# Optimization experiments

Measured on AMD Instinct MI355X. Metric: run time of the kernel, lower is better.

## Reference

```python
import jax, jax.numpy as jnp
import numpy as np
import math

N_USER = 50000
N_ITEM = 50000
E_PER = 400000
F_IN = 128
F_OUT = 128
H = 4
D = F_OUT // H  # 32
NUM_ET = 2  # edge types: 0 = user->item, 1 = item->user


def setup_inputs() -> dict:
    key = jax.random.key(0)
    ks = jax.random.split(key, 16)
    s = 0.05  # weight scale to keep activations tame
    return {
        "x_user": jax.random.normal(ks[0], (N_USER, F_IN), jnp.float32),
        "x_item": jax.random.normal(ks[1], (N_ITEM, F_IN), jnp.float32),
        "W_kqv_user": jax.random.normal(ks[2], (F_IN, 3 * F_OUT), jnp.float32) * s,
        "b_kqv_user": jax.random.normal(ks[3], (3 * F_OUT,), jnp.float32) * s,
        "W_kqv_item": jax.random.normal(ks[4], (F_IN, 3 * F_OUT), jnp.float32) * s,
        "b_kqv_item": jax.random.normal(ks[5], (3 * F_OUT,), jnp.float32) * s,
        "Wk_rel": jax.random.normal(ks[6], (H * NUM_ET, D, D), jnp.float32) * s,
        "Wv_rel": jax.random.normal(ks[7], (H * NUM_ET, D, D), jnp.float32) * s,
        "W_out_user": jax.random.normal(ks[8], (F_OUT, F_OUT), jnp.float32) * s,
        "b_out_user": jax.random.normal(ks[9], (F_OUT,), jnp.float32) * s,
        "W_out_item": jax.random.normal(ks[10], (F_OUT, F_OUT), jnp.float32) * s,
        "b_out_item": jax.random.normal(ks[11], (F_OUT,), jnp.float32) * s,
        "skip_user": jnp.ones((1,), jnp.float32),
        "skip_item": jnp.ones((1,), jnp.float32),
        "p_rel_ui": jnp.ones((H,), jnp.float32),
        "p_rel_iu": jnp.ones((H,), jnp.float32),
        "edge_ui": jax.random.randint(ks[12], (2, E_PER), 0, N_USER, dtype=jnp.int32),
        "edge_iu": jax.random.randint(ks[13], (2, E_PER), 0, N_ITEM, dtype=jnp.int32),
    }


def _kqv(x, W, b):
    o = x @ W + b  # [N, 3F]
    k, q, v = o[:, :F_OUT], o[:, F_OUT:2 * F_OUT], o[:, 2 * F_OUT:]
    return (k.reshape(-1, H, D), q.reshape(-1, H, D), v.reshape(-1, H, D))


def _rel(x, Wrel, et):
    # HeteroLinear with type index h*NUM_ET + et per head (is_sorted layout)
    W = Wrel[jnp.arange(H) * NUM_ET + et]  # [H, D, D]
    return jnp.einsum('nhd,hde->nhe', x, W)


def reference(x_user, x_item, W_kqv_user, b_kqv_user, W_kqv_item, b_kqv_item,
              Wk_rel, Wv_rel, W_out_user, b_out_user, W_out_item, b_out_item,
              skip_user, skip_item, p_rel_ui, p_rel_iu, edge_ui, edge_iu):
    ku, qu, vu = _kqv(x_user, W_kqv_user, b_kqv_user)
    ki, qi, vi = _kqv(x_item, W_kqv_item, b_kqv_item)

    # per-edge-type relation transform of K/V (grouped GEMM by head x edge-type)
    k0, v0 = _rel(ku, Wk_rel, 0), _rel(vu, Wv_rel, 0)  # src of user->item
    k1, v1 = _rel(ki, Wk_rel, 1), _rel(vi, Wv_rel, 1)  # src of item->user

    q_all = jnp.concatenate([qu, qi], 0)  # dst offsets: user=0, item=N_USER
    n_tot = N_USER + N_ITEM

    src0, dst0 = edge_ui[0], edge_ui[1] + N_USER
    src1, dst1 = edge_iu[0], edge_iu[1]

    kj = jnp.concatenate([k0[src0], k1[src1]], 0)  # [E, H, D]
    vj = jnp.concatenate([v0[src0], v1[src1]], 0)  # [E, H, D]
    dst = jnp.concatenate([dst0, dst1], 0)         # [E]
    p = jnp.concatenate([jnp.broadcast_to(p_rel_ui, (E_PER, H)),
                         jnp.broadcast_to(p_rel_iu, (E_PER, H))], 0)

    qe = q_all[dst]                                  # [E, H, D]
    alpha = (qe * kj).sum(-1) * p / math.sqrt(D)     # [E, H]

    # segment softmax over destination nodes (PyG softmax: max-shift, +1e-16)
    amax = jax.ops.segment_max(alpha, dst, num_segments=n_tot)
    a = jnp.exp(alpha - amax[dst])
    denom = jax.ops.segment_sum(a, dst, num_segments=n_tot)
    a = a / (denom[dst] + 1e-16)

    out = jax.ops.segment_sum(vj * a[:, :, None], dst, num_segments=n_tot)
    out = out.reshape(n_tot, F_OUT)
    out_u, out_i = out[:N_USER], out[N_USER:]

    g = lambda t: jax.nn.gelu(t, approximate=False)
    a_u = g(out_u) @ W_out_user + b_out_user
    a_i = g(out_i) @ W_out_item + b_out_item

    su = jax.nn.sigmoid(skip_user)  # out_channels == in_channels -> skip blend
    si = jax.nn.sigmoid(skip_item)
    return (su * a_u + (1.0 - su) * x_user,
            si * a_i + (1.0 - si) * x_item)
```

## Files before the change

kernel.cpp:

```cpp
#include <hip/hip_runtime.h>
#include <hip/hip_bf16.h>
#include <math.h>

#define N_USERS 50000
#define N_ITEMS 50000
#define NN      100000
#define E_PER_  400000
#define E_TOT   800000
#define FDIM    128
#define NH      4
#define HD      32
#define SCAN_CHUNK 1024
#define SCAN_NB    ((NN + SCAN_CHUNK - 1) / SCAN_CHUNK)
#define KQV_NB  ((N_USERS + 127) / 128)

typedef _Float16 h2 __attribute__((ext_vector_type(2)));
typedef _Float16 h8 __attribute__((ext_vector_type(8)));
typedef __attribute__((ext_vector_type(4))) float f32x4;

__device__ __forceinline__ float gelu_exact(float x) {
    return 0.5f * x * (1.0f + erff(x * 0.70710678118654752f));
}
__device__ __forceinline__ unsigned short f2h_bits(float f) {
    _Float16 h = (_Float16)f;
    union { _Float16 h; unsigned short u; } c; c.h = h; return c.u;
}
__device__ __forceinline__ h2 pkrtz(float a, float b) {
    return __builtin_bit_cast(h2, __builtin_amdgcn_cvt_pkrtz(a, b));
}
__device__ __forceinline__ unsigned h2_as_u(h2 x) {
    union { h2 h; unsigned u; } c; c.h = x; return c.u;
}
__device__ __forceinline__ h2 u_as_h2(unsigned x) {
    union { h2 h; unsigned u; } c; c.u = x; return c.h;
}
__device__ __forceinline__ h2 shfl_h2(h2 x, int m) {
    return u_as_h2((unsigned)__shfl_xor((int)h2_as_u(x), m));
}
__device__ __forceinline__ size_t wfrag_idx(int n, int k) {
    int ch = n >> 7, nt = (n >> 4) & 7, lr = n & 15;
    int ks = k >> 5, lg = (k >> 3) & 3, e = k & 7;
    return ((size_t)(((ch * 8 + nt) * 4 + ks) * 64 + lg * 16 + lr)) * 8 + e;
}

__global__ void prep_kqv(
    const float* __restrict__ W_u, const float* __restrict__ b_u,
    const float* __restrict__ W_i, const float* __restrict__ b_i,
    const float* __restrict__ Wk_rel, const float* __restrict__ Wv_rel,
    unsigned short* __restrict__ F_u, float* __restrict__ bias_u,
    unsigned short* __restrict__ F_i, float* __restrict__ bias_i)
{
    const int et = blockIdx.x >= 384;
    const int n = blockIdx.x - et * 384;
    const int k = threadIdx.x;
    const float* W = et ? W_i : W_u;
    const float* b = et ? b_i : b_u;
    unsigned short* F = et ? F_i : F_u;
    float* bias_f = et ? bias_i : bias_u;
    float s;
    if (n < 128) {
        int h = n >> 5, e = n & 31;
        const float* wr = Wk_rel + (size_t)(h * 2 + et) * 1024 + e;
        const float* wc = W + (size_t)k * 384 + h * 32;
        s = 0.f;
        for (int d = 0; d < 32; ++d) s = fmaf(wc[d], wr[d * 32], s);
        if (k == 0) {
            float bs = 0.f;
            for (int d = 0; d < 32; ++d) bs = fmaf(b[h * 32 + d], wr[d * 32], bs);
            bias_f[n] = bs;
        }
    } else if (n < 256) {
        s = W[(size_t)k * 384 + n];
        if (k == 0) bias_f[n] = b[n];
    } else {
        int h = (n - 256) >> 5, e = (n - 256) & 31;
        const float* wr = Wv_rel + (size_t)(h * 2 + et) * 1024 + e;
        const float* wc = W + (size_t)k * 384 + 256 + h * 32;
        s = 0.f;
        for (int d = 0; d < 32; ++d) s = fmaf(wc[d], wr[d * 32], s);
        if (k == 0) {
            float bs = 0.f;
            for (int d = 0; d < 32; ++d) bs = fmaf(b[256 + h * 32 + d], wr[d * 32], bs);
            bias_f[n] = bs;
        }
    }
    F[wfrag_idx(n, k)] = f2h_bits(s);
}

__global__ void prep_wo(
    const float* __restrict__ W_u, unsigned short* __restrict__ F_u,
    const float* __restrict__ W_i, unsigned short* __restrict__ F_i)
{
    int i = blockIdx.x * blockDim.x + threadIdx.x;
    int side = i >= 128 * 128;
    int j = i - side * 128 * 128;
    if (j >= 128 * 128) return;
    int n = j >> 7, k = j & 127;
    const float* W = side ? W_i : W_u;
    unsigned short* F = side ? F_i : F_u;
    F[wfrag_idx(n, k)] = f2h_bits(W[(size_t)k * 128 + n]);
}

__global__ __launch_bounds__(256, 3) void kqv_mfma(
    const float* __restrict__ X_u, const unsigned short* __restrict__ F_u,
    const float* __restrict__ bias_u,
    const float* __restrict__ X_i, const unsigned short* __restrict__ F_i,
    const float* __restrict__ bias_i,
    unsigned short* __restrict__ kk_b,
    unsigned short* __restrict__ q_b,
    unsigned short* __restrict__ vv_b)
{
    const int t = threadIdx.x;
    const int side = blockIdx.x >= KQV_NB;
    const int m0 = (blockIdx.x - side * KQV_NB) * 128;
    const float* X = side ? X_i : X_u;
    const unsigned short* F = side ? F_i : F_u;
    const float* bias = side ? bias_i : bias_u;
    const int side_off = side ? N_USERS : 0;
    const int M = N_USERS;

    const int wave = t >> 6, lane = t & 63;
    const int lr = lane & 15, lg = lane >> 4;
    const int rbase = m0 + wave * 32;

    h8 am[2][4];
    #pragma unroll
    for (int mt = 0; mt < 2; ++mt)
        #pragma unroll
        for (int ks = 0; ks < 4; ++ks) {
            int row = rbase + mt * 16 + lr;
            float4 a = make_float4(0.f, 0.f, 0.f, 0.f);
            float4 b4 = make_float4(0.f, 0.f, 0.f, 0.f);
            if (row < M) {
                const float* px = X + (size_t)row * 128 + ks * 32 + lg * 8;
                a  = *reinterpret_cast<const float4*>(px);
                b4 = *reinterpret_cast<const float4*>(px + 4);
            }
            union { h2 q[4]; h8 f; } u;
            u.q[0] = pkrtz(a.x, a.y);
            u.q[1] = pkrtz(a.z, a.w);
            u.q[2] = pkrtz(b4.x, b4.y);
            u.q[3] = pkrtz(b4.z, b4.w);
            am[mt][ks] = u.f;
        }

    #pragma unroll
    for (int ch = 0; ch < 3; ++ch) {
        f32x4 acc[2][8];
        const f32x4 zero = {0.f, 0.f, 0.f, 0.f};
        #pragma unroll
        for (int mt = 0; mt < 2; ++mt)
            #pragma unroll
            for (int nt = 0; nt < 8; ++nt) acc[mt][nt] = zero;

        h8 bc[4], bn[4];
        #pragma unroll
        for (int ks = 0; ks < 4; ++ks)
            bc[ks] = *reinterpret_cast<const h8*>(
                F + ((size_t)((ch * 8 + 0) * 4 + ks) * 64 + lane) * 8);

        #pragma unroll
        for (int nt = 0; nt < 8; ++nt) {
            if (nt < 7) {
                #pragma unroll
                for (int ks = 0; ks < 4; ++ks)
                    bn[ks] = *reinterpret_cast<const h8*>(
                        F + ((size_t)((ch * 8 + nt + 1) * 4 + ks) * 64 + lane) * 8);
            }
            #pragma unroll
            for (int mt = 0; mt < 2; ++mt)
                #pragma unroll
                for (int ks = 0; ks < 4; ++ks)
                    acc[mt][nt] = __builtin_amdgcn_mfma_f32_16x16x32_f16(
                        bc[ks], am[mt][ks], acc[mt][nt], 0, 0, 0);
            #pragma unroll
            for (int ks = 0; ks < 4; ++ks) bc[ks] = bn[ks];
        }

        unsigned short* arr = (ch == 0) ? kk_b : (ch == 1) ? q_b : vv_b;
        #pragma unroll
        for (int nt = 0; nt < 8; ++nt) {
            float4 bv = *reinterpret_cast<const float4*>(bias + ch * 128 + nt * 16 + lg * 4);
            #pragma unroll
            for (int mt = 0; mt < 2; ++mt) {
                int row = rbase + mt * 16 + lr;
                if (row < M) {
                    h2 lo = pkrtz(acc[mt][nt][0] + bv.x, acc[mt][nt][1] + bv.y);
                    h2 hi = pkrtz(acc[mt][nt][2] + bv.z, acc[mt][nt][3] + bv.w);
                    uint2 st = make_uint2(h2_as_u(lo), h2_as_u(hi));
                    *reinterpret_cast<uint2*>(
                        arr + (size_t)(side_off + row) * 128 + nt * 16 + lg * 4) = st;
                }
            }
        }
    }
}

__device__ __forceinline__ void edge_src_dst(
    int e, const int* __restrict__ edge_ui, const int* __restrict__ edge_iu,
    int& src, int& dst)
{
    if (e < E_PER_) {
        src = edge_ui[e];
        dst = edge_ui[E_PER_ + e] + N_USERS;
    } else {
        int e2 = e - E_PER_;
        src = N_USERS + edge_iu[e2];
        dst = edge_iu[E_PER_ + e2];
    }
}

__global__ __launch_bounds__(256) void hist_kernel(
    const int* __restrict__ edge_ui, const int* __restrict__ edge_iu,
    int* __restrict__ cnt)
{
    int e = blockIdx.x * blockDim.x + threadIdx.x;
    if (e >= E_TOT) return;
    int src, dst;
    edge_src_dst(e, edge_ui, edge_iu, src, dst);
    atomicAdd(cnt + dst, 1);
}

__global__ __launch_bounds__(256) void scan1_kernel(
    const int* __restrict__ cnt, int* __restrict__ base, int* __restrict__ bsum)
{
    __shared__ int ssum[256];
    const int t = threadIdx.x;
    const int i0 = blockIdx.x * SCAN_CHUNK + t * 4;
    int v[4];
    #pragma unroll
    for (int j = 0; j < 4; ++j) v[j] = (i0 + j < NN) ? cnt[i0 + j] : 0;
    int tsum = v[0] + v[1] + v[2] + v[3];
    ssum[t] = tsum;
    __syncthreads();
    int run = tsum;
    for (int off = 1; off < 256; off <<= 1) {
        int o = (t >= off) ? ssum[t - off] : 0;
        __syncthreads();
        run += o;
        ssum[t] = run;
        __syncthreads();
    }
    int excl = run - tsum;
    int p = excl;
    #pragma unroll
    for (int j = 0; j < 4; ++j) {
        if (i0 + j < NN) base[i0 + j] = p;
        p += v[j];
    }
    if (t == 255) bsum[blockIdx.x] = run;
}

__global__ __launch_bounds__(256) void scan3_kernel(
    const int* __restrict__ base, const int* __restrict__ bsum,
    const int* __restrict__ cnt,
    int* __restrict__ cursor, int2* __restrict__ meta2)
{
    const int lane = threadIdx.x & 63;
    const int chunk = blockIdx.x >> 2;
    int v0 = (lane < chunk) ? bsum[lane] : 0;
    int v1 = (64 + lane < chunk && 64 + lane < SCAN_NB) ? bsum[64 + lane] : 0;
    int s = v0 + v1;
    #pragma unroll
    for (int off = 1; off < 64; off <<= 1) s += __shfl_xor(s, off);
    int i = blockIdx.x * 256 + threadIdx.x;
    if (i < NN) {
        int b = base[i] + s;
        cursor[i] = b;
        meta2[i] = make_int2(b, cnt[i]);
    }
}

__global__ __launch_bounds__(256) void fill_kernel(
    const int* __restrict__ edge_ui, const int* __restrict__ edge_iu,
    int* __restrict__ cursor, int* __restrict__ esrc)
{
    int e = blockIdx.x * blockDim.x + threadIdx.x;
    if (e >= E_TOT) return;
    int src, dst;
    edge_src_dst(e, edge_ui, edge_iu, src, dst);
    int pos = atomicAdd(cursor + dst, 1);
    esrc[pos] = src;
}

__global__ __launch_bounds__(256) void attn_fused(
    const unsigned short* __restrict__ q_b, const unsigned short* __restrict__ kk_b,
    const unsigned short* __restrict__ vv_b,
    const int2* __restrict__ meta2, const int* __restrict__ esrc,
    const float* __restrict__ p_ui, const float* __restrict__ p_iu,
    unsigned short* __restrict__ oa)
{
    const int wid  = (blockIdx.x * blockDim.x + threadIdx.x) >> 6;
    const int lane = threadIdx.x & 63;
    const int nw   = (gridDim.x * blockDim.x) >> 6;
    const int g    = lane >> 4;
    const int p    = lane & 15;
    const int h    = p >> 2;
    const float rsd = 0.17677669529663687f;
    const float pu = p_ui[h], pi = p_iu[h];

    for (int n = wid; n < NN; n += nw) {
        const float pr = (n >= N_USERS) ? pu : pi;
        union { uint4 u; h2 h[4]; } qu;
        qu.u = *reinterpret_cast<const uint4*>(q_b + (size_t)n * 128 + p * 8);
        float l = 0.f;
        h2 acc2[4];
        #pragma unroll
        for (int i = 0; i < 4; ++i) acc2[i] = (h2)(_Float16)0;
        const int2 mt = meta2[n];
        const int s0 = mt.x, c = mt.y;

        if (c > 0) {
            bool valid = g < c;
            int src = esrc[s0 + (valid ? g : 0)];
            uint4 k4 = *reinterpret_cast<const uint4*>(kk_b + (size_t)src * 128 + p * 8);
            uint4 v4 = *reinterpret_cast<const uint4*>(vv_b + (size_t)src * 128 + p * 8);

            for (int j = 0; j < c; j += 4) {
                uint4 k4n, v4n;
                bool validn = false;
                if (j + 4 < c) {
                    int jn = j + 4 + g;
                    validn = jn < c;
                    int srcn = esrc[s0 + (validn ? jn : 0)];
                    k4n = *reinterpret_cast<const uint4*>(kk_b + (size_t)srcn * 128 + p * 8);
                    v4n = *reinterpret_cast<const uint4*>(vv_b + (size_t)srcn * 128 + p * 8);
                }

                union { uint4 u; h2 h[4]; } ku, vu;
                ku.u = k4; vu.u = v4;
                float s = 0.f;
                s = __builtin_amdgcn_fdot2(qu.h[0], ku.h[0], s, false);
                s = __builtin_amdgcn_fdot2(qu.h[1], ku.h[1], s, false);
                s = __builtin_amdgcn_fdot2(qu.h[2], ku.h[2], s, false);
                s = __builtin_amdgcn_fdot2(qu.h[3], ku.h[3], s, false);
                s += __shfl_xor(s, 1);
                s += __shfl_xor(s, 2);
                float w = valid ? __expf(s * pr * rsd) : 0.f;
                l += w;
                h2 wpk = pkrtz(w, w);
                #pragma unroll
                for (int i = 0; i < 4; ++i) acc2[i] += vu.h[i] * wpk;

                k4 = k4n; v4 = v4n; valid = validn;
            }
        }

        l += __shfl_xor(l, 16); l += __shfl_xor(l, 32);

        const bool b1 = (g & 2) != 0;
        h2 r4[2];
        #pragma unroll
        for (int i = 0; i < 2; ++i) {
            h2 mine = b1 ? acc2[2 + i] : acc2[i];
            h2 send = b1 ? acc2[i] : acc2[2 + i];
            r4[i] = mine + shfl_h2(send, 32);
        }
        const bool b0 = (g & 1) != 0;
        h2 mine = b0 ? r4[1] : r4[0];
        h2 send = b0 ? r4[0] : r4[1];
        h2 r2 = mine + shfl_h2(send, 16);
        float inv = 1.0f / (l + 1e-16f);
        float o0 = gelu_exact((float)r2[0] * inv);
        float o1 = gelu_exact((float)r2[1] * inv);
        unsigned pk = h2_as_u(pkrtz(o0, o1));
        *reinterpret_cast<unsigned*>(oa + (size_t)n * 128 + p * 8 + 2 * g) = pk;
    }
}

__global__ __launch_bounds__(256, 3) void final_mfma(
    const unsigned short* __restrict__ oa,
    const float* __restrict__ x_u, const unsigned short* __restrict__ F_u,
    const float* __restrict__ bo_u, const float* __restrict__ skip_u,
    const float* __restrict__ x_i, const unsigned short* __restrict__ F_i,
    const float* __restrict__ bo_i, const float* __restrict__ skip_i,
    float* __restrict__ out)
{
    const int t = threadIdx.x;
    const int side = blockIdx.x >= KQV_NB;
    const int m0 = (blockIdx.x - side * KQV_NB) * 128;
    const float* x = side ? x_i : x_u;
    const unsigned short* F = side ? F_i : F_u;
    const float* bo = side ? bo_i : bo_u;
    const float* skip = side ? skip_i : skip_u;
    const int row_off = side ? N_USERS : 0;
    const int M = N_USERS;

    const int wave = t >> 6, lane = t & 63;
    const int lr = lane & 15, lg = lane >> 4;
    const int rbase = m0 + wave * 32;

    h8 am[2][4];
    const h8 bz = {0, 0, 0, 0, 0, 0, 0, 0};
    #pragma unroll
    for (int mt = 0; mt < 2; ++mt)
        #pragma unroll
        for (int ks = 0; ks < 4; ++ks) {
            int row = rbase + mt * 16 + lr;
            am[mt][ks] = (row < M)
                ? *reinterpret_cast<const h8*>(
                      oa + (size_t)(row_off + row) * 128 + ks * 32 + lg * 8)
                : bz;
        }

    f32x4 acc[2][8];
    const f32x4 zero = {0.f, 0.f, 0.f, 0.f};
    #pragma unroll
    for (int mt = 0; mt < 2; ++mt)
        #pragma unroll
        for (int nt = 0; nt < 8; ++nt) acc[mt][nt] = zero;

    h8 bc[4], bn[4];
    #pragma unroll
    for (int ks = 0; ks < 4; ++ks)
        bc[ks] = *reinterpret_cast<const h8*>(
            F + ((size_t)(0 * 4 + ks) * 64 + lane) * 8);

    #pragma unroll
    for (int nt = 0; nt < 8; ++nt) {
        if (nt < 7) {
            #pragma unroll
            for (int ks = 0; ks < 4; ++ks)
                bn[ks] = *reinterpret_cast<const h8*>(
                    F + ((size_t)((nt + 1) * 4 + ks) * 64 + lane) * 8);
        }
        #pragma unroll
        for (int mt = 0; mt < 2; ++mt)
            #pragma unroll
            for (int ks = 0; ks < 4; ++ks)
                acc[mt][nt] = __builtin_amdgcn_mfma_f32_16x16x32_f16(
                    bc[ks], am[mt][ks], acc[mt][nt], 0, 0, 0);
        #pragma unroll
        for (int ks = 0; ks < 4; ++ks) bc[ks] = bn[ks];
    }

    const float sg = 1.0f / (1.0f + expf(-skip[0]));
    #pragma unroll
    for (int nt = 0; nt < 8; ++nt) {
        float4 bv = *reinterpret_cast<const float4*>(bo + nt * 16 + lg * 4);
        #pragma unroll
        for (int mt = 0; mt < 2; ++mt) {
            int row = rbase + mt * 16 + lr;
            if (row < M) {
                float4 xv = *reinterpret_cast<const float4*>(
                    x + (size_t)row * 128 + nt * 16 + lg * 4);
                float4 res;
                res.x = sg * (acc[mt][nt][0] + bv.x) + (1.f - sg) * xv.x;
                res.y = sg * (acc[mt][nt][1] + bv.y) + (1.f - sg) * xv.y;
                res.z = sg * (acc[mt][nt][2] + bv.z) + (1.f - sg) * xv.z;
                res.w = sg * (acc[mt][nt][3] + bv.w) + (1.f - sg) * xv.w;
                *reinterpret_cast<float4*>(
                    out + (size_t)(row_off + row) * 128 + nt * 16 + lg * 4) = res;
            }
        }
    }
}

extern "C" void kernel_launch(void* const* d_in, const int* in_sizes, int n_in,
                              void* d_out, int out_size, void* d_ws, size_t ws_size,
                              hipStream_t stream)
{
    const float* x_user     = (const float*)d_in[0];
    const float* x_item     = (const float*)d_in[1];
    const float* W_kqv_user = (const float*)d_in[2];
    const float* b_kqv_user = (const float*)d_in[3];
    const float* W_kqv_item = (const float*)d_in[4];
    const float* b_kqv_item = (const float*)d_in[5];
    const float* Wk_rel     = (const float*)d_in[6];
    const float* Wv_rel     = (const float*)d_in[7];
    const float* W_out_user = (const float*)d_in[8];
    const float* b_out_user = (const float*)d_in[9];
    const float* W_out_item = (const float*)d_in[10];
    const float* b_out_item = (const float*)d_in[11];
    const float* skip_user  = (const float*)d_in[12];
    const float* skip_item  = (const float*)d_in[13];
    const float* p_ui       = (const float*)d_in[14];
    const float* p_iu       = (const float*)d_in[15];
    const int*   edge_ui    = (const int*)d_in[16];
    const int*   edge_iu    = (const int*)d_in[17];

    const size_t NODE_F = (size_t)NN * FDIM;
    char* w = (char*)d_ws;
    size_t off = 0;
    auto alloc = [&](size_t bytes) {
        char* p = w + off;
        off += (bytes + 255) & ~(size_t)255;
        return p;
    };
    unsigned short* q_b   = (unsigned short*)alloc(NODE_F * 2);
    unsigned short* kk_b  = (unsigned short*)alloc(NODE_F * 2);
    unsigned short* vv_b  = (unsigned short*)alloc(NODE_F * 2);
    unsigned short* oa_b  = (unsigned short*)alloc(NODE_F * 2);
    int* esrc   = (int*)alloc((size_t)E_TOT * 4);
    int* cnt    = (int*)alloc((size_t)NN * 4);
    int* base   = (int*)alloc((size_t)NN * 4);
    int* cursor = (int*)alloc((size_t)NN * 4);
    int* bsum   = (int*)alloc((size_t)SCAN_NB * 4);
    int2* meta2 = (int2*)alloc((size_t)NN * 8);
    unsigned short* F_u    = (unsigned short*)alloc(384 * 128 * 2);
    unsigned short* F_i    = (unsigned short*)alloc(384 * 128 * 2);
    float*          bias_u = (float*)alloc(384 * 4);
    float*          bias_i = (float*)alloc(384 * 4);
    unsigned short* Fo_u   = (unsigned short*)alloc(128 * 128 * 2);
    unsigned short* Fo_i   = (unsigned short*)alloc(128 * 128 * 2);

    prep_kqv<<<768, 128, 0, stream>>>(W_kqv_user, b_kqv_user, W_kqv_item, b_kqv_item,
                                      Wk_rel, Wv_rel, F_u, bias_u, F_i, bias_i);
    prep_wo<<<128, 256, 0, stream>>>(W_out_user, Fo_u, W_out_item, Fo_i);

    kqv_mfma<<<2 * KQV_NB, 256, 0, stream>>>(x_user, F_u, bias_u,
                                             x_item, F_i, bias_i,
                                             kk_b, q_b, vv_b);

    hipMemsetAsync(cnt, 0, (size_t)NN * 4, stream);
    hist_kernel<<<(E_TOT + 255) / 256, 256, 0, stream>>>(edge_ui, edge_iu, cnt);
    scan1_kernel<<<SCAN_NB, 256, 0, stream>>>(cnt, base, bsum);
    scan3_kernel<<<(NN + 255) / 256, 256, 0, stream>>>(base, bsum, cnt, cursor, meta2);
    fill_kernel<<<(E_TOT + 255) / 256, 256, 0, stream>>>(edge_ui, edge_iu, cursor, esrc);

    attn_fused<<<2048, 256, 0, stream>>>(q_b, kk_b, vv_b, meta2, esrc,
                                         p_ui, p_iu, oa_b);

    final_mfma<<<2 * KQV_NB, 256, 0, stream>>>(
        oa_b, x_user, Fo_u, b_out_user, skip_user,
        x_item, Fo_i, b_out_item, skip_item, (float*)d_out);
}
```

Before: 236.0 us.

## Fuse prep kernels and memset, fold histogram into KQV GEMM, pair nodes in attention

The two weight-prep kernels and the count memset are merged into one launch, and the destination histogram is computed inside the KQV MFMA kernel instead of its own kernel. Together these cut launch count and let the histogram atomics overlap with the GEMM. The attention kernel now has each wave process a user node and an item node together, interleaving their gathers to raise memory-level parallelism. The cost is more register pressure and divergence when the two nodes have different degrees, and the GEMM kernel now carries extra atomic work.

```diff
diff --git a/kernel.cpp b/kernel.cpp
--- a/kernel.cpp
+++ b/kernel.cpp
@@ -5,6 +5,7 @@
 #define N_USERS 50000
 #define N_ITEMS 50000
 #define NN      100000
+#define HN      50000
 #define E_PER_  400000
 #define E_TOT   800000
 #define FDIM    128
@@ -43,62 +44,81 @@
     return ((size_t)(((ch * 8 + nt) * 4 + ks) * 64 + lg * 16 + lr)) * 8 + e;
 }
 
-__global__ void prep_kqv(
+__global__ void prep_all(
     const float* __restrict__ W_u, const float* __restrict__ b_u,
     const float* __restrict__ W_i, const float* __restrict__ b_i,
     const float* __restrict__ Wk_rel, const float* __restrict__ Wv_rel,
     unsigned short* __restrict__ F_u, float* __restrict__ bias_u,
-    unsigned short* __restrict__ F_i, float* __restrict__ bias_i)
-{
-    const int et = blockIdx.x >= 384;
-    const int n = blockIdx.x - et * 384;
-    const int k = threadIdx.x;
-    const float* W = et ? W_i : W_u;
-    const float* b = et ? b_i : b_u;
-    unsigned short* F = et ? F_i : F_u;
-    float* bias_f = et ? bias_i : bias_u;
-    float s;
-    if (n < 128) {
-        int h = n >> 5, e = n & 31;
-        const float* wr = Wk_rel + (size_t)(h * 2 + et) * 1024 + e;
-        const float* wc = W + (size_t)k * 384 + h * 32;
-        s = 0.f;
-        for (int d = 0; d < 32; ++d) s = fmaf(wc[d], wr[d * 32], s);
-        if (k == 0) {
-            float bs = 0.f;
-            for (int d = 0; d < 32; ++d) bs = fmaf(b[h * 32 + d], wr[d * 32], bs);
-            bias_f[n] = bs;
-        }
-    } else if (n < 256) {
-        s = W[(size_t)k * 384 + n];
-        if (k == 0) bias_f[n] = b[n];
+    unsigned short* __restrict__ F_i, float* __restrict__ bias_i,
+    const float* __restrict__ Wo_u, unsigned short* __restrict__ Fo_u,
+    const float* __restrict__ Wo_i, unsigned short* __restrict__ Fo_i,
+    int* __restrict__ cnt)
+{
+    const int bid = blockIdx.x;
+    if (bid < 768) {
+        const int et = bid >= 384;
+        const int n = bid - et * 384;
+        const int k = threadIdx.x;
+        const float* W = et ? W_i : W_u;
+        const float* b = et ? b_i : b_u;
+        unsigned short* F = et ? F_i : F_u;
+        float* bias_f = et ? bias_i : bias_u;
+        float s;
+        if (n < 128) {
+            int h = n >> 5, e = n & 31;
+            const float* wr = Wk_rel + (size_t)(h * 2 + et) * 1024 + e;
+            const float* wc = W + (size_t)k * 384 + h * 32;
+            s = 0.f;
+            for (int d = 0; d < 32; ++d) s = fmaf(wc[d], wr[d * 32], s);
+            if (k == 0) {
+                float bs = 0.f;
+                for (int d = 0; d < 32; ++d) bs = fmaf(b[h * 32 + d], wr[d * 32], bs);
+                bias_f[n] = bs;
+            }
+        } else if (n < 256) {
+            s = W[(size_t)k * 384 + n];
+            if (k == 0) bias_f[n] = b[n];
+        } else {
+            int h = (n - 256) >> 5, e = (n - 256) & 31;
+            const float* wr = Wv_rel + (size_t)(h * 2 + et) * 1024 + e;
+            const float* wc = W + (size_t)k * 384 + 256 + h * 32;
+            s = 0.f;
+            for (int d = 0; d < 32; ++d) s = fmaf(wc[d], wr[d * 32], s);
+            if (k == 0) {
+                float bs = 0.f;
+                for (int d = 0; d < 32; ++d) bs = fmaf(b[256 + h * 32 + d], wr[d * 32], bs);
+                bias_f[n] = bs;
+            }
+        }
+        F[wfrag_idx(n, k)] = f2h_bits(s);
+    } else if (bid < 1024) {
+        int i = (bid - 768) * 128 + threadIdx.x;
+        int side = i >= 16384;
+        int j = i - side * 16384;
+        int n = j >> 7, k = j & 127;
+        const float* W = side ? Wo_i : Wo_u;
+        unsigned short* F = side ? Fo_i : Fo_u;
+        F[wfrag_idx(n, k)] = f2h_bits(W[(size_t)k * 128 + n]);
     } else {
-        int h = (n - 256) >> 5, e = (n - 256) & 31;
-        const float* wr = Wv_rel + (size_t)(h * 2 + et) * 1024 + e;
-        const float* wc = W + (size_t)k * 384 + 256 + h * 32;
-        s = 0.f;
-        for (int d = 0; d < 32; ++d) s = fmaf(wc[d], wr[d * 32], s);
-        if (k == 0) {
-            float bs = 0.f;
-            for (int d = 0; d < 32; ++d) bs = fmaf(b[256 + h * 32 + d], wr[d * 32], bs);
-            bias_f[n] = bs;
-        }
-    }
-    F[wfrag_idx(n, k)] = f2h_bits(s);
-}
-
-__global__ void prep_wo(
-    const float* __restrict__ W_u, unsigned short* __restrict__ F_u,
-    const float* __restrict__ W_i, unsigned short* __restrict__ F_i)
-{
-    int i = blockIdx.x * blockDim.x + threadIdx.x;
-    int side = i >= 128 * 128;
-    int j = i - side * 128 * 128;
-    if (j >= 128 * 128) return;
-    int n = j >> 7, k = j & 127;
-    const float* W = side ? W_i : W_u;
-    unsigned short* F = side ? F_i : F_u;
-    F[wfrag_idx(n, k)] = f2h_bits(W[(size_t)k * 128 + n]);
+        int i = (bid - 1024) * 512 + threadIdx.x * 4;
+        #pragma unroll
+        for (int j = 0; j < 4; ++j)
+            if (i + j < NN) cnt[i + j] = 0;
+    }
+}
+
+__device__ __forceinline__ void edge_src_dst(
+    int e, const int* __restrict__ edge_ui, const int* __restrict__ edge_iu,
+    int& src, int& dst)
+{
+    if (e < E_PER_) {
+        src = edge_ui[e];
+        dst = edge_ui[E_PER_ + e] + N_USERS;
+    } else {
+        int e2 = e - E_PER_;
+        src = N_USERS + edge_iu[e2];
+        dst = edge_iu[E_PER_ + e2];
+    }
 }
 
 __global__ __launch_bounds__(256, 3) void kqv_mfma(
@@ -108,9 +128,18 @@
     const float* __restrict__ bias_i,
     unsigned short* __restrict__ kk_b,
     unsigned short* __restrict__ q_b,
-    unsigned short* __restrict__ vv_b)
+    unsigned short* __restrict__ vv_b,
+    const int* __restrict__ edge_ui, const int* __restrict__ edge_iu,
+    int* __restrict__ cnt)
 {
     const int t = threadIdx.x;
+
+    for (int e = blockIdx.x * 256 + t; e < E_TOT; e += gridDim.x * 256) {
+        int src, dst;
+        edge_src_dst(e, edge_ui, edge_iu, src, dst);
+        atomicAdd(cnt + dst, 1);
+    }
+
     const int side = blockIdx.x >= KQV_NB;
     const int m0 = (blockIdx.x - side * KQV_NB) * 128;
     const float* X = side ? X_i : X_u;
@@ -196,31 +225,6 @@
     }
 }
 
-__device__ __forceinline__ void edge_src_dst(
-    int e, const int* __restrict__ edge_ui, const int* __restrict__ edge_iu,
-    int& src, int& dst)
-{
-    if (e < E_PER_) {
-        src = edge_ui[e];
-        dst = edge_ui[E_PER_ + e] + N_USERS;
-    } else {
-        int e2 = e - E_PER_;
-        src = N_USERS + edge_iu[e2];
-        dst = edge_iu[E_PER_ + e2];
-    }
-}
-
-__global__ __launch_bounds__(256) void hist_kernel(
-    const int* __restrict__ edge_ui, const int* __restrict__ edge_iu,
-    int* __restrict__ cnt)
-{
-    int e = blockIdx.x * blockDim.x + threadIdx.x;
-    if (e >= E_TOT) return;
-    int src, dst;
-    edge_src_dst(e, edge_ui, edge_iu, src, dst);
-    atomicAdd(cnt + dst, 1);
-}
-
 __global__ __launch_bounds__(256) void scan1_kernel(
     const int* __restrict__ cnt, int* __restrict__ base, int* __restrict__ bsum)
 {
@@ -297,74 +301,117 @@
     const int p    = lane & 15;
     const int h    = p >> 2;
     const float rsd = 0.17677669529663687f;
-    const float pu = p_ui[h], pi = p_iu[h];
-
-    for (int n = wid; n < NN; n += nw) {
-        const float pr = (n >= N_USERS) ? pu : pi;
-        union { uint4 u; h2 h[4]; } qu;
-        qu.u = *reinterpret_cast<const uint4*>(q_b + (size_t)n * 128 + p * 8);
-        float l = 0.f;
-        h2 acc2[4];
-        #pragma unroll
-        for (int i = 0; i < 4; ++i) acc2[i] = (h2)(_Float16)0;
-        const int2 mt = meta2[n];
-        const int s0 = mt.x, c = mt.y;
-
-        if (c > 0) {
-            bool valid = g < c;
-            int src = esrc[s0 + (valid ? g : 0)];
-            uint4 k4 = *reinterpret_cast<const uint4*>(kk_b + (size_t)src * 128 + p * 8);
-            uint4 v4 = *reinterpret_cast<const uint4*>(vv_b + (size_t)src * 128 + p * 8);
-
-            for (int j = 0; j < c; j += 4) {
-                uint4 k4n, v4n;
-                bool validn = false;
-                if (j + 4 < c) {
-                    int jn = j + 4 + g;
-                    validn = jn < c;
-                    int srcn = esrc[s0 + (validn ? jn : 0)];
-                    k4n = *reinterpret_cast<const uint4*>(kk_b + (size_t)srcn * 128 + p * 8);
-                    v4n = *reinterpret_cast<const uint4*>(vv_b + (size_t)srcn * 128 + p * 8);
-                }
-
+    const float pr1 = p_iu[h] * rsd;
+    const float pr2 = p_ui[h] * rsd;
+    const int EC = E_TOT - 1;
+
+    for (int n = wid; n < HN; n += nw) {
+        const int n2 = n + HN;
+        const int2 mt1 = meta2[n];
+        const int2 mt2 = meta2[n2];
+        union { uint4 u; h2 h[4]; } qu1, qu2;
+        qu1.u = *reinterpret_cast<const uint4*>(q_b + (size_t)n  * 128 + p * 8);
+        qu2.u = *reinterpret_cast<const uint4*>(q_b + (size_t)n2 * 128 + p * 8);
+        float l1 = 0.f, l2 = 0.f;
+        h2 a1[4], a2[4];
+        #pragma unroll
+        for (int i = 0; i < 4; ++i) { a1[i] = (h2)(_Float16)0; a2[i] = (h2)(_Float16)0; }
+        const int s01 = mt1.x, c1 = mt1.y;
+        const int s02 = mt2.x, c2 = mt2.y;
+
+        bool val1 = g < c1, val2 = g < c2;
+        int sr1 = esrc[min(s01 + (val1 ? g : 0), EC)];
+        int sr2 = esrc[min(s02 + (val2 ? g : 0), EC)];
+        uint4 k41 = *reinterpret_cast<const uint4*>(kk_b + (size_t)sr1 * 128 + p * 8);
+        uint4 v41 = *reinterpret_cast<const uint4*>(vv_b + (size_t)sr1 * 128 + p * 8);
+        uint4 k42 = *reinterpret_cast<const uint4*>(kk_b + (size_t)sr2 * 128 + p * 8);
+        uint4 v42 = *reinterpret_cast<const uint4*>(vv_b + (size_t)sr2 * 128 + p * 8);
+
+        for (int j = 0; j < c1 || j < c2; j += 4) {
+            uint4 k41n, v41n, k42n, v42n;
+            bool v1n = false, v2n = false;
+            if (j + 4 < c1) {
+                int jn = j + 4 + g;
+                v1n = jn < c1;
+                int srn = esrc[s01 + (v1n ? jn : 0)];
+                k41n = *reinterpret_cast<const uint4*>(kk_b + (size_t)srn * 128 + p * 8);
+                v41n = *reinterpret_cast<const uint4*>(vv_b + (size_t)srn * 128 + p * 8);
+            }
+            if (j + 4 < c2) {
+                int jn = j + 4 + g;
+                v2n = jn < c2;
+                int srn = esrc[s02 + (v2n ? jn : 0)];
+                k42n = *reinterpret_cast<const uint4*>(kk_b + (size_t)srn * 128 + p * 8);
+                v42n = *reinterpret_cast<const uint4*>(vv_b + (size_t)srn * 128 + p * 8);
+            }
+
+            if (j < c1) {
                 union { uint4 u; h2 h[4]; } ku, vu;
-                ku.u = k4; vu.u = v4;
+                ku.u = k41; vu.u = v41;
                 float s = 0.f;
-                s = __builtin_amdgcn_fdot2(qu.h[0], ku.h[0], s, false);
-                s = __builtin_amdgcn_fdot2(qu.h[1], ku.h[1], s, false);
-                s = __builtin_amdgcn_fdot2(qu.h[2], ku.h[2], s, false);
-                s = __builtin_amdgcn_fdot2(qu.h[3], ku.h[3], s, false);
+                s = __builtin_amdgcn_fdot2(qu1.h[0], ku.h[0], s, false);
+                s = __builtin_amdgcn_fdot2(qu1.h[1], ku.h[1], s, false);
+                s = __builtin_amdgcn_fdot2(qu1.h[2], ku.h[2], s, false);
+                s = __builtin_amdgcn_fdot2(qu1.h[3], ku.h[3], s, false);
                 s += __shfl_xor(s, 1);
                 s += __shfl_xor(s, 2);
-                float w = valid ? __expf(s * pr * rsd) : 0.f;
-                l += w;
+                float w = val1 ? __expf(s * pr1) : 0.f;
+                l1 += w;
                 h2 wpk = pkrtz(w, w);
                 #pragma unroll
-                for (int i = 0; i < 4; ++i) acc2[i] += vu.h[i] * wpk;
-
-                k4 = k4n; v4 = v4n; valid = validn;
-            }
-        }
-
-        l += __shfl_xor(l, 16); l += __shfl_xor(l, 32);
+                for (int i = 0; i < 4; ++i) a1[i] += vu.h[i] * wpk;
+            }
+            if (j < c2) {
+                union { uint4 u; h2 h[4]; } ku, vu;
+                ku.u = k42; vu.u = v42;
+                float s = 0.f;
+                s = __builtin_amdgcn_fdot2(qu2.h[0], ku.h[0], s, false);
+                s = __builtin_amdgcn_fdot2(qu2.h[1], ku.h[1], s, false);
+                s = __builtin_amdgcn_fdot2(qu2.h[2], ku.h[2], s, false);
+                s = __builtin_amdgcn_fdot2(qu2.h[3], ku.h[3], s, false);
+                s += __shfl_xor(s, 1);
+                s += __shfl_xor(s, 2);
+                float w = val2 ? __expf(s * pr2) : 0.f;
+                l2 += w;
+                h2 wpk = pkrtz(w, w);
+                #pragma unroll
+                for (int i = 0; i < 4; ++i) a2[i] += vu.h[i] * wpk;
+            }
+
+            k41 = k41n; v41 = v41n; val1 = v1n;
+            k42 = k42n; v42 = v42n; val2 = v2n;
+        }
+
+        l1 += __shfl_xor(l1, 16); l1 += __shfl_xor(l1, 32);
+        l2 += __shfl_xor(l2, 16); l2 += __shfl_xor(l2, 32);
 
         const bool b1 = (g & 2) != 0;
-        h2 r4[2];
+        h2 r41[2], r42[2];
         #pragma unroll
         for (int i = 0; i < 2; ++i) {
-            h2 mine = b1 ? acc2[2 + i] : acc2[i];
-            h2 send = b1 ? acc2[i] : acc2[2 + i];
-            r4[i] = mine + shfl_h2(send, 32);
+            h2 m1 = b1 ? a1[2 + i] : a1[i];
+            h2 s1 = b1 ? a1[i] : a1[2 + i];
+            r41[i] = m1 + shfl_h2(s1, 32);
+            h2 m2 = b1 ? a2[2 + i] : a2[i];
+            h2 s2 = b1 ? a2[i] : a2[2 + i];
+            r42[i] = m2 + shfl_h2(s2, 32);
         }
         const bool b0 = (g & 1) != 0;
-        h2 mine = b0 ? r4[1] : r4[0];
-        h2 send = b0 ? r4[0] : r4[1];
-        h2 r2 = mine + shfl_h2(send, 16);
-        float inv = 1.0f / (l + 1e-16f);
-        float o0 = gelu_exact((float)r2[0] * inv);
-        float o1 = gelu_exact((float)r2[1] * inv);
-        unsigned pk = h2_as_u(pkrtz(o0, o1));
-        *reinterpret_cast<unsigned*>(oa + (size_t)n * 128 + p * 8 + 2 * g) = pk;
+        h2 m1 = b0 ? r41[1] : r41[0];
+        h2 s1 = b0 ? r41[0] : r41[1];
+        h2 r21 = m1 + shfl_h2(s1, 16);
+        h2 m2 = b0 ? r42[1] : r42[0];
+        h2 s2 = b0 ? r42[0] : r42[1];
+        h2 r22 = m2 + shfl_h2(s2, 16);
+
+        float inv1 = 1.0f / (l1 + 1e-16f);
+        float inv2 = 1.0f / (l2 + 1e-16f);
+        unsigned pk1 = h2_as_u(pkrtz(gelu_exact((float)r21[0] * inv1),
+                                     gelu_exact((float)r21[1] * inv1)));
+        unsigned pk2 = h2_as_u(pkrtz(gelu_exact((float)r22[0] * inv2),
+                                     gelu_exact((float)r22[1] * inv2)));
+        *reinterpret_cast<unsigned*>(oa + (size_t)n  * 128 + p * 8 + 2 * g) = pk1;
+        *reinterpret_cast<unsigned*>(oa + (size_t)n2 * 128 + p * 8 + 2 * g) = pk2;
     }
 }
 
@@ -504,16 +551,17 @@
     unsigned short* Fo_u   = (unsigned short*)alloc(128 * 128 * 2);
     unsigned short* Fo_i   = (unsigned short*)alloc(128 * 128 * 2);
 
-    prep_kqv<<<768, 128, 0, stream>>>(W_kqv_user, b_kqv_user, W_kqv_item, b_kqv_item,
-                                      Wk_rel, Wv_rel, F_u, bias_u, F_i, bias_i);
-    prep_wo<<<128, 256, 0, stream>>>(W_out_user, Fo_u, W_out_item, Fo_i);
+    const int ZB = (NN + 511) / 512;
+    prep_all<<<1024 + ZB, 128, 0, stream>>>(
+        W_kqv_user, b_kqv_user, W_kqv_item, b_kqv_item, Wk_rel, Wv_rel,
+        F_u, bias_u, F_i, bias_i,
+        W_out_user, Fo_u, W_out_item, Fo_i, cnt);
 
     kqv_mfma<<<2 * KQV_NB, 256, 0, stream>>>(x_user, F_u, bias_u,
                                              x_item, F_i, bias_i,
-                                             kk_b, q_b, vv_b);
-
-    hipMemsetAsync(cnt, 0, (size_t)NN * 4, stream);
-    hist_kernel<<<(E_TOT + 255) / 256, 256, 0, stream>>>(edge_ui, edge_iu, cnt);
+                                             kk_b, q_b, vv_b,
+                                             edge_ui, edge_iu, cnt);
+
     scan1_kernel<<<SCAN_NB, 256, 0, stream>>>(cnt, base, bsum);
     scan3_kernel<<<(NN + 255) / 256, 256, 0, stream>>>(base, bsum, cnt, cursor, meta2);
     fill_kernel<<<(E_TOT + 255) / 256, 256, 0, stream>>>(edge_ui, edge_iu, cursor, esrc);
```

Result: no change. 236.8 us (+0.4%).
